# Performance work log

Hardware: AMD Instinct MI355X
Metric: run time of the kernel (lower is better)

Reference implementation:

```python
import jax, jax.numpy as jnp
import numpy as np

B, S, D, O = 8, 2048, 1024, 1024  # batch, seq_len, state_dim(=input_dim), output_dim


def setup_inputs() -> dict:
    key = jax.random.key(0)
    k_in, k_a, k_bc = jax.random.split(key, 3)
    inputs = jax.random.normal(k_in, (B, S, D), dtype=jnp.float32)
    # Stable diagonal transition (|A| < 1) so the 2048-step recurrence stays bounded.
    A = jax.random.uniform(k_a, (D,), minval=-0.99, maxval=0.99, dtype=jnp.float32)
    BC = jax.random.normal(k_bc, (D, O), dtype=jnp.float32) / D
    return {"inputs": inputs, "A": A, "BC": BC}


def reference(inputs, A, BC):
    # Diagonal LTI recurrence: h_t = A * h_{t-1} + x_t ; out_t = h_t @ BC
    # h0 = zeros (the module's h0 Parameter is initialized to zeros).
    x_tfirst = jnp.swapaxes(inputs, 0, 1)  # [S, B, D]

    def step(h, x_t):
        h = h * A + x_t
        return h, h

    h0 = jnp.zeros((inputs.shape[0], A.shape[0]), dtype=inputs.dtype)
    _, hs = jax.lax.scan(step, h0, x_tfirst)  # hs: [S, B, D]
    # Single fused projection over all timesteps instead of per-step matmuls.
    out = jnp.einsum('sbd,do->bso', hs, BC)  # [B, S, O]
    return out
```

## Files before the change

### kernel.cpp

```cpp
#include <hip/hip_runtime.h>
#include <hip/hip_bf16.h>

#define BB 8
#define SS 2048
#define DD 1024
#define OO 1024
#define MM (BB * SS)
#define KK DD
#define NN OO
#define CC 64
#define LL 32

typedef __bf16 bf16x8 __attribute__((ext_vector_type(8)));
typedef __bf16 bf16x2 __attribute__((ext_vector_type(2)));
typedef float floatx4 __attribute__((ext_vector_type(4)));

__device__ __forceinline__ float2 fma2(float2 h, float2 a, float2 v) {
    h.x = fmaf(h.x, a.x, v.x);
    h.y = fmaf(h.y, a.y, v.y);
    return h;
}

__global__ __launch_bounds__(512) void prep(const float* __restrict__ x,
                                            const float* __restrict__ A,
                                            float* __restrict__ carry,
                                            const float* __restrict__ BC,
                                            __bf16* __restrict__ BCt) {
    __shared__ float tile[32][33];
    const int id = blockIdx.x;
    if (id < BB * CC) {
        const int c = id & (CC - 1);
        const int b = id >> 6;
        const int i2 = threadIdx.x;
        const float2 a = ((const float2*)A)[i2];
        const float2* xp = (const float2*)(x + ((size_t)b * SS + (size_t)c * LL) * DD) + i2;
        float2 h = make_float2(0.f, 0.f);
#pragma unroll
        for (int t0 = 0; t0 < LL; t0 += 8) {
            float2 v[8];
#pragma unroll
            for (int u = 0; u < 8; ++u) v[u] = xp[(size_t)(t0 + u) * (DD / 2)];
#pragma unroll
            for (int u = 0; u < 8; ++u) h = fma2(h, a, v[u]);
        }
        ((float2*)carry)[((size_t)b * CC + c) * (DD / 2) + i2] = h;
    } else {
        const int t = id - BB * CC;
        const int o0 = (t & 31) * 32;
        const int d0 = (t >> 5) * 32;
        const int tx = threadIdx.x & 31;
        const int ty = threadIdx.x >> 5;
#pragma unroll
        for (int i = 0; i < 2; ++i) {
            const int dd = ty + i * 16;
            tile[dd][tx] = BC[(size_t)(d0 + dd) * OO + o0 + tx];
        }
        __syncthreads();
#pragma unroll
        for (int i = 0; i < 2; ++i) {
            const int oo = ty + i * 16;
            BCt[(size_t)(o0 + oo) * DD + d0 + tx] = (__bf16)tile[tx][oo];
        }
    }
}

__global__ __launch_bounds__(512) void scan_emit(const float* __restrict__ x,
                                                 const float* __restrict__ A,
                                                 const float* __restrict__ carry,
                                                 __bf16* __restrict__ hs) {
    const int id = blockIdx.x;
    const int c = id & (CC - 1);
    const int b = id >> 6;
    const int i2 = threadIdx.x;
    const float2 a = ((const float2*)A)[i2];
    float2 aL = a;
#pragma unroll
    for (int i = 0; i < 5; ++i) { aL.x *= aL.x; aL.y *= aL.y; }
    float2 h = make_float2(0.f, 0.f);
    const float2* cp = (const float2*)carry + (size_t)b * CC * (DD / 2) + i2;
    int j = 0;
    for (; j + 8 <= c; j += 8) {
        float2 cv[8];
#pragma unroll
        for (int u = 0; u < 8; ++u) cv[u] = cp[(size_t)(j + u) * (DD / 2)];
#pragma unroll
        for (int u = 0; u < 8; ++u) h = fma2(h, aL, cv[u]);
    }
    for (; j < c; ++j) h = fma2(h, aL, cp[(size_t)j * (DD / 2)]);

    const size_t base = ((size_t)b * SS + (size_t)c * LL) * DD;
    const float2* xp = (const float2*)(x + base) + i2;
    bf16x2* hp = (bf16x2*)(hs + base) + i2;
#pragma unroll
    for (int t0 = 0; t0 < LL; t0 += 8) {
        float2 v[8];
#pragma unroll
        for (int u = 0; u < 8; ++u) v[u] = xp[(size_t)(t0 + u) * (DD / 2)];
#pragma unroll
        for (int u = 0; u < 8; ++u) {
            h = fma2(h, a, v[u]);
            bf16x2 o;
            o[0] = (__bf16)h.x; o[1] = (__bf16)h.y;
            hp[(size_t)(t0 + u) * (DD / 2)] = o;
        }
    }
}

#define GTM 256
#define GTN 256
#define GTK 64
#define GNT (KK / GTK)

__device__ __forceinline__ void async16(void* lds, const void* g) {
    __builtin_amdgcn_global_load_lds(
        (__attribute__((address_space(1))) void*)(void*)g,
        (__attribute__((address_space(3))) void*)lds, 16, 0, 0);
}

#define MEMFENCE asm volatile("" ::: "memory")
#define BARRIER do { MEMFENCE; __builtin_amdgcn_s_barrier(); MEMFENCE; } while (0)
#define VMCNT0 asm volatile("s_waitcnt vmcnt(0)" ::: "memory")

__global__ __launch_bounds__(512, 2) void gemm_bt(const __bf16* __restrict__ Am,
                                                  const __bf16* __restrict__ Bt,
                                                  float* __restrict__ C) {
    __shared__ __align__(16) __bf16 As[2][GTM * GTK];
    __shared__ __align__(16) __bf16 Bs[2][GTN * GTK];

    const int tid = threadIdx.x;
    const int wave = tid >> 6;
    const int lane = tid & 63;
    const int wm = (wave >> 2) * 128;
    const int wn = (wave & 3) * 64;
    const int lanelo = lane & 15;
    const int quad = lane >> 4;

    const int bid = blockIdx.x;
    const int xcd = bid & 7;
    const int loc = bid >> 3;
    const int tile_m = (xcd * 8 + (loc >> 2)) * GTM;
    const int tile_n = (loc & 3) * GTN;

    const __bf16* gsrc[4][2];
    int ldsoff[4][2];
#pragma unroll
    for (int a = 0; a < 2; ++a)
#pragma unroll
        for (int u = 0; u < 2; ++u) {
            const int idx = a * 1024 + u * 512 + tid;
            const int rho = idx >> 3, qs = idx & 7;
            const int rl = rho & 127;
            const int r = (rl >> 6) * 128 + a * 64 + (rl & 63);
            const int qg = qs ^ (rho & 7);
            gsrc[a * 3][u] = Am + (size_t)(tile_m + r) * KK + qg * 8;
            ldsoff[a * 3][u] = idx * 8;
        }
#pragma unroll
    for (int b = 0; b < 2; ++b)
#pragma unroll
        for (int u = 0; u < 2; ++u) {
            const int idx = b * 1024 + u * 512 + tid;
            const int rho = idx >> 3, qs = idx & 7;
            const int rl = rho & 127;
            const int r = (rl >> 5) * 64 + b * 32 + (rl & 31);
            const int qg = qs ^ (rho & 7);
            gsrc[1 + b][u] = Bt + (size_t)(tile_n + r) * KK + qg * 8;
            ldsoff[1 + b][u] = idx * 8;
        }

    auto stage = [&](int p, int bufi, int koff) {
        __bf16* base = (p == 0 || p == 3) ? As[bufi] : Bs[bufi];
#pragma unroll
        for (int u = 0; u < 2; ++u)
            async16(base + ldsoff[p][u], gsrc[p][u] + koff);
    };

    floatx4 acc[8][4];
#pragma unroll
    for (int i = 0; i < 8; ++i)
#pragma unroll
        for (int j = 0; j < 4; ++j) acc[i][j] = (floatx4){0.f, 0.f, 0.f, 0.f};

    bf16x8 af[4][2];
    bf16x8 bv[2][2][2];

    auto read_a = [&](const __bf16* as, int mh) {
#pragma unroll
        for (int il = 0; il < 4; ++il)
#pragma unroll
            for (int kk = 0; kk < 2; ++kk) {
                const int rho = mh * 128 + (wm >> 1) + il * 16 + lanelo;
                af[il][kk] = *(const bf16x8*)(as + rho * 64 + (((kk * 4 + quad) ^ (lanelo & 7)) * 8));
            }
    };
    auto read_b = [&](const __bf16* bs, int nh) {
#pragma unroll
        for (int jl = 0; jl < 2; ++jl)
#pragma unroll
            for (int kk = 0; kk < 2; ++kk) {
                const int rho = nh * 128 + (wn >> 1) + jl * 16 + lanelo;
                bv[nh][jl][kk] = *(const bf16x8*)(bs + rho * 64 + (((kk * 4 + quad) ^ (lanelo & 7)) * 8));
            }
    };
    auto mfma16 = [&](int mh, int nh) {
        __builtin_amdgcn_s_setprio(1);
#pragma unroll
        for (int il = 0; il < 4; ++il)
#pragma unroll
            for (int jl = 0; jl < 2; ++jl)
#pragma unroll
                for (int kk = 0; kk < 2; ++kk)
                    acc[mh * 4 + il][nh * 2 + jl] = __builtin_amdgcn_mfma_f32_16x16x32_bf16(
                        af[il][kk], bv[nh][jl][kk], acc[mh * 4 + il][nh * 2 + jl], 0, 0, 0);
        __builtin_amdgcn_s_setprio(0);
    };
    auto store_q = [&](int mh, int nh) {
#pragma unroll
        for (int il = 0; il < 4; ++il) {
            const int row = tile_m + wm + (mh * 4 + il) * 16 + quad * 4;
#pragma unroll
            for (int r = 0; r < 4; ++r) {
                float* crow = C + (size_t)(row + r) * NN + tile_n + wn + lanelo;
#pragma unroll
                for (int jl = 0; jl < 2; ++jl)
                    crow[(nh * 2 + jl) * 16] = acc[mh * 4 + il][nh * 2 + jl][r];
            }
        }
    };

    stage(0, 0, 0);
    stage(3, 0, 0);
    stage(1, 0, 0);
    stage(2, 0, 0);

    for (int t = 0; t < GNT - 1; ++t) {
        const int cur = t & 1, nxt = cur ^ 1;
        const __bf16* as = As[cur];
        const __bf16* bs = Bs[cur];
        const int ko = (t + 1) * GTK;

        VMCNT0;
        BARRIER;

        stage(0, nxt, ko);
        stage(3, nxt, ko);
        stage(1, nxt, ko);
        stage(2, nxt, ko);

        read_a(as, 0);
        read_b(bs, 0);
        mfma16(0, 0);

        read_b(bs, 1);
        mfma16(0, 1);

        read_a(as, 1);
        mfma16(1, 1);

        mfma16(1, 0);
    }

    {
        const __bf16* as = As[(GNT - 1) & 1];
        const __bf16* bs = Bs[(GNT - 1) & 1];
        VMCNT0;
        BARRIER;
        read_a(as, 0);
        read_b(bs, 0);
        mfma16(0, 0);
        read_b(bs, 1);
        mfma16(0, 1);
        store_q(0, 0);
        read_a(as, 1);
        mfma16(1, 1);
        store_q(0, 1);
        mfma16(1, 0);
        store_q(1, 0);
        store_q(1, 1);
    }
}

extern "C" void kernel_launch(void* const* d_in, const int* in_sizes, int n_in,
                              void* d_out, int out_size, void* d_ws, size_t ws_size,
                              hipStream_t stream) {
    const float* x  = (const float*)d_in[0];
    const float* A  = (const float*)d_in[1];
    const float* BC = (const float*)d_in[2];
    float* out = (float*)d_out;

    char* ws = (char*)d_ws;
    __bf16* hs   = (__bf16*)ws;
    float* carry = (float*)(ws + 33554432);
    __bf16* BCt  = (__bf16*)(ws + 33554432 + 2097152);

    prep<<<dim3(BB * CC + 1024), 512, 0, stream>>>(x, A, carry, BC, BCt);
    scan_emit<<<dim3(BB * CC), 512, 0, stream>>>(x, A, carry, hs);
    gemm_bt<<<dim3(MM / GTM * (NN / GTN)), 512, 0, stream>>>(hs, BCt, out);
}
```

Before: 166.7 us.

## Fuse chunk-carry and scan-emit kernels with inter-block flag synchronization

Merges the prep and scan_emit kernels into one launch. Each chunk block computes its local carry, publishes a flag, then spin-waits on the flags of earlier chunks in the same batch before combining carries and emitting hs. The BC transpose blocks now handle four tiles each. This removes one kernel launch and keeps the x chunk warm in cache between the two passes, at the cost of spin-waiting, a reliance on all 512 scan blocks being co-resident to avoid deadlock, and a memset of flags placed in the output buffer.

```diff
diff --git a/kernel.cpp b/kernel.cpp
--- a/kernel.cpp
+++ b/kernel.cpp
@@ -21,58 +21,69 @@
     return h;
 }
 
-__global__ __launch_bounds__(512) void prep(const float* __restrict__ x,
-                                            const float* __restrict__ A,
-                                            float* __restrict__ carry,
-                                            const float* __restrict__ BC,
-                                            __bf16* __restrict__ BCt) {
+__global__ __launch_bounds__(512) void scan_fused(const float* __restrict__ x,
+                                                  const float* __restrict__ A,
+                                                  float* __restrict__ carry,
+                                                  const float* __restrict__ BC,
+                                                  __bf16* __restrict__ BCt,
+                                                  __bf16* __restrict__ hs,
+                                                  unsigned int* __restrict__ flags) {
     __shared__ float tile[32][33];
     const int id = blockIdx.x;
-    if (id < BB * CC) {
-        const int c = id & (CC - 1);
-        const int b = id >> 6;
-        const int i2 = threadIdx.x;
-        const float2 a = ((const float2*)A)[i2];
-        const float2* xp = (const float2*)(x + ((size_t)b * SS + (size_t)c * LL) * DD) + i2;
-        float2 h = make_float2(0.f, 0.f);
-#pragma unroll
-        for (int t0 = 0; t0 < LL; t0 += 8) {
-            float2 v[8];
-#pragma unroll
-            for (int u = 0; u < 8; ++u) v[u] = xp[(size_t)(t0 + u) * (DD / 2)];
-#pragma unroll
-            for (int u = 0; u < 8; ++u) h = fma2(h, a, v[u]);
-        }
-        ((float2*)carry)[((size_t)b * CC + c) * (DD / 2) + i2] = h;
-    } else {
-        const int t = id - BB * CC;
-        const int o0 = (t & 31) * 32;
-        const int d0 = (t >> 5) * 32;
+    if (id >= BB * CC) {
         const int tx = threadIdx.x & 31;
         const int ty = threadIdx.x >> 5;
 #pragma unroll
-        for (int i = 0; i < 2; ++i) {
-            const int dd = ty + i * 16;
-            tile[dd][tx] = BC[(size_t)(d0 + dd) * OO + o0 + tx];
-        }
-        __syncthreads();
-#pragma unroll
-        for (int i = 0; i < 2; ++i) {
-            const int oo = ty + i * 16;
-            BCt[(size_t)(o0 + oo) * DD + d0 + tx] = (__bf16)tile[tx][oo];
-        }
-    }
-}
-
-__global__ __launch_bounds__(512) void scan_emit(const float* __restrict__ x,
-                                                 const float* __restrict__ A,
-                                                 const float* __restrict__ carry,
-                                                 __bf16* __restrict__ hs) {
-    const int id = blockIdx.x;
+        for (int w = 0; w < 4; ++w) {
+            const int t = (id - BB * CC) * 4 + w;
+            const int o0 = (t & 31) * 32;
+            const int d0 = (t >> 5) * 32;
+            __syncthreads();
+#pragma unroll
+            for (int i = 0; i < 2; ++i) {
+                const int dd = ty + i * 16;
+                tile[dd][tx] = BC[(size_t)(d0 + dd) * OO + o0 + tx];
+            }
+            __syncthreads();
+#pragma unroll
+            for (int i = 0; i < 2; ++i) {
+                const int oo = ty + i * 16;
+                BCt[(size_t)(o0 + oo) * DD + d0 + tx] = (__bf16)tile[tx][oo];
+            }
+        }
+        return;
+    }
+
     const int c = id & (CC - 1);
     const int b = id >> 6;
     const int i2 = threadIdx.x;
     const float2 a = ((const float2*)A)[i2];
+    const size_t base = ((size_t)b * SS + (size_t)c * LL) * DD;
+    const float2* xp = (const float2*)(x + base) + i2;
+
+    {
+        float2 h = make_float2(0.f, 0.f);
+#pragma unroll
+        for (int t0 = 0; t0 < LL; t0 += 8) {
+            float2 v[8];
+#pragma unroll
+            for (int u = 0; u < 8; ++u) v[u] = xp[(size_t)(t0 + u) * (DD / 2)];
+#pragma unroll
+            for (int u = 0; u < 8; ++u) h = fma2(h, a, v[u]);
+        }
+        ((float2*)carry)[((size_t)b * CC + c) * (DD / 2) + i2] = h;
+    }
+    __threadfence();
+    __syncthreads();
+    if (threadIdx.x == 0) atomicExch(&flags[id], 1u);
+
+    if ((int)threadIdx.x < c) {
+        while (atomicAdd(&flags[(b << 6) + threadIdx.x], 0u) == 0u)
+            __builtin_amdgcn_s_sleep(2);
+    }
+    __syncthreads();
+    __threadfence();
+
     float2 aL = a;
 #pragma unroll
     for (int i = 0; i < 5; ++i) { aL.x *= aL.x; aL.y *= aL.y; }
@@ -88,8 +99,6 @@
     }
     for (; j < c; ++j) h = fma2(h, aL, cp[(size_t)j * (DD / 2)]);
 
-    const size_t base = ((size_t)b * SS + (size_t)c * LL) * DD;
-    const float2* xp = (const float2*)(x + base) + i2;
     bf16x2* hp = (bf16x2*)(hs + base) + i2;
 #pragma unroll
     for (int t0 = 0; t0 < LL; t0 += 8) {
@@ -293,7 +302,9 @@
     float* carry = (float*)(ws + 33554432);
     __bf16* BCt  = (__bf16*)(ws + 33554432 + 2097152);
 
-    prep<<<dim3(BB * CC + 1024), 512, 0, stream>>>(x, A, carry, BC, BCt);
-    scan_emit<<<dim3(BB * CC), 512, 0, stream>>>(x, A, carry, hs);
+    unsigned int* flags = (unsigned int*)d_out;
+    hipMemsetAsync(flags, 0, BB * CC * sizeof(unsigned int), stream);
+
+    scan_fused<<<dim3(BB * CC + 256), 512, 0, stream>>>(x, A, carry, BC, BCt, hs, flags);
     gemm_bt<<<dim3(MM / GTM * (NN / GTN)), 512, 0, stream>>>(hs, BCt, out);
 }
```

Result: slower. 425.3 us (+155.1%).

## Restructure GEMM main loop into finer-grained interleaved load/compute stages

Applied to the files above, without the earlier changes.

Replaces the per-K-tile full vmcnt(0) wait and single barrier with a schedule that splits each tile's global-to-LDS staging into four quarter loads. These are interleaved with the four MFMA quadrants, using partial vmcnt waits, extra barriers and sched_barrier fences. Quarter loads for the tile after next go into the current buffer once its parts are consumed, so loads run about 1.5 tiles ahead. The aim is to hide global load latency behind MFMA work, at the cost of many more barriers per iteration and a fragile correctness argument about buffer reuse.

```diff
diff --git a/kernel.cpp b/kernel.cpp
--- a/kernel.cpp
+++ b/kernel.cpp
@@ -119,7 +119,11 @@
 
 #define MEMFENCE asm volatile("" ::: "memory")
 #define BARRIER do { MEMFENCE; __builtin_amdgcn_s_barrier(); MEMFENCE; } while (0)
+#define VMCNT6 asm volatile("s_waitcnt vmcnt(6)" ::: "memory")
+#define VMCNT4 asm volatile("s_waitcnt vmcnt(4)" ::: "memory")
 #define VMCNT0 asm volatile("s_waitcnt vmcnt(0)" ::: "memory")
+#define LGKM0  asm volatile("s_waitcnt lgkmcnt(0)" ::: "memory")
+#define SCHED0 __builtin_amdgcn_sched_barrier(0)
 
 __global__ __launch_bounds__(512, 2) void gemm_bt(const __bf16* __restrict__ Am,
                                                   const __bf16* __restrict__ Bt,
@@ -229,35 +233,82 @@
     };
 
     stage(0, 0, 0);
+    stage(2, 0, 0);
+    stage(1, 0, 0);
     stage(3, 0, 0);
-    stage(1, 0, 0);
-    stage(2, 0, 0);
-
-    for (int t = 0; t < GNT - 1; ++t) {
-        const int cur = t & 1, nxt = cur ^ 1;
-        const __bf16* as = As[cur];
-        const __bf16* bs = Bs[cur];
-        const int ko = (t + 1) * GTK;
-
-        VMCNT0;
-        BARRIER;
-
-        stage(0, nxt, ko);
-        stage(3, nxt, ko);
-        stage(1, nxt, ko);
-        stage(2, nxt, ko);
-
+    stage(0, 1, GTK);
+    stage(2, 1, GTK);
+    VMCNT4;
+    BARRIER;
+
+    for (int t = 0; t < GNT - 2; ++t) {
+        const int cb = t & 1, nb = cb ^ 1;
+        const __bf16* as = As[cb];
+        const __bf16* bs = Bs[cb];
+        const int ko1 = (t + 1) * GTK;
+        const int ko2 = (t + 2) * GTK;
+
+        stage(1, nb, ko1);
         read_a(as, 0);
         read_b(bs, 0);
+        VMCNT6; BARRIER;
+        LGKM0; SCHED0;
         mfma16(0, 0);
-
+        BARRIER;
+
+        stage(3, nb, ko1);
         read_b(bs, 1);
+        VMCNT6; BARRIER;
+        LGKM0; SCHED0;
         mfma16(0, 1);
-
+        BARRIER;
+
+        stage(0, cb, ko2);
         read_a(as, 1);
+        VMCNT6; BARRIER;
+        LGKM0; SCHED0;
         mfma16(1, 1);
-
+        BARRIER;
+
+        stage(2, cb, ko2);
+        VMCNT6; BARRIER;
+        SCHED0;
         mfma16(1, 0);
+        BARRIER;
+    }
+
+    {
+        const int t = GNT - 2;
+        const int cb = t & 1, nb = cb ^ 1;
+        const __bf16* as = As[cb];
+        const __bf16* bs = Bs[cb];
+        const int ko1 = (t + 1) * GTK;
+
+        stage(1, nb, ko1);
+        read_a(as, 0);
+        read_b(bs, 0);
+        VMCNT6; BARRIER;
+        LGKM0; SCHED0;
+        mfma16(0, 0);
+        BARRIER;
+
+        stage(3, nb, ko1);
+        read_b(bs, 1);
+        VMCNT6; BARRIER;
+        LGKM0; SCHED0;
+        mfma16(0, 1);
+        BARRIER;
+
+        read_a(as, 1);
+        VMCNT6; BARRIER;
+        LGKM0; SCHED0;
+        mfma16(1, 1);
+        BARRIER;
+
+        VMCNT6; BARRIER;
+        SCHED0;
+        mfma16(1, 0);
+        BARRIER;
     }
 
     {
@@ -267,11 +318,14 @@
         BARRIER;
         read_a(as, 0);
         read_b(bs, 0);
+        LGKM0; SCHED0;
         mfma16(0, 0);
         read_b(bs, 1);
+        LGKM0; SCHED0;
         mfma16(0, 1);
         store_q(0, 0);
         read_a(as, 1);
+        LGKM0; SCHED0;
         mfma16(1, 1);
         store_q(0, 1);
         mfma16(1, 0);
```

Result: slower. 172.0 us (+3.1%).

## Fuse chunk scan into GEMM A-tile staging, drop bf16 hs buffer

Applied to the files above, without the earlier changes.

The materialized bf16 hidden-state tensor is removed. A small kernel now writes only the per-chunk starting states. Inside the GEMM, each wave loads 32 timesteps of fp32 input for a 64-wide K slice, runs the recurrence in registers and writes bf16 values straight into the swizzled LDS A tile. This avoids writing and re-reading the 32MB hs buffer, but each of the four N-tile blocks per M tile now re-reads fp32 x (twice the bytes of the bf16 hs) and redoes the scan. The scan runs as synchronous loads in the GEMM loop instead of async staging, which may stall MFMA issue.

```diff
diff --git a/kernel.cpp b/kernel.cpp
--- a/kernel.cpp
+++ b/kernel.cpp
@@ -12,7 +12,6 @@
 #define LL 32
 
 typedef __bf16 bf16x8 __attribute__((ext_vector_type(8)));
-typedef __bf16 bf16x2 __attribute__((ext_vector_type(2)));
 typedef float floatx4 __attribute__((ext_vector_type(4)));
 
 __device__ __forceinline__ float2 fma2(float2 h, float2 a, float2 v) {
@@ -64,10 +63,9 @@
     }
 }
 
-__global__ __launch_bounds__(512) void scan_emit(const float* __restrict__ x,
-                                                 const float* __restrict__ A,
-                                                 const float* __restrict__ carry,
-                                                 __bf16* __restrict__ hs) {
+__global__ __launch_bounds__(512) void prefix_k(const float* __restrict__ A,
+                                                const float* __restrict__ carry,
+                                                float* __restrict__ P) {
     const int id = blockIdx.x;
     const int c = id & (CC - 1);
     const int b = id >> 6;
@@ -87,23 +85,7 @@
         for (int u = 0; u < 8; ++u) h = fma2(h, aL, cv[u]);
     }
     for (; j < c; ++j) h = fma2(h, aL, cp[(size_t)j * (DD / 2)]);
-
-    const size_t base = ((size_t)b * SS + (size_t)c * LL) * DD;
-    const float2* xp = (const float2*)(x + base) + i2;
-    bf16x2* hp = (bf16x2*)(hs + base) + i2;
-#pragma unroll
-    for (int t0 = 0; t0 < LL; t0 += 8) {
-        float2 v[8];
-#pragma unroll
-        for (int u = 0; u < 8; ++u) v[u] = xp[(size_t)(t0 + u) * (DD / 2)];
-#pragma unroll
-        for (int u = 0; u < 8; ++u) {
-            h = fma2(h, a, v[u]);
-            bf16x2 o;
-            o[0] = (__bf16)h.x; o[1] = (__bf16)h.y;
-            hp[(size_t)(t0 + u) * (DD / 2)] = o;
-        }
-    }
+    ((float2*)P)[(size_t)id * (DD / 2) + i2] = h;
 }
 
 #define GTM 256
@@ -120,8 +102,11 @@
 #define MEMFENCE asm volatile("" ::: "memory")
 #define BARRIER do { MEMFENCE; __builtin_amdgcn_s_barrier(); MEMFENCE; } while (0)
 #define VMCNT0 asm volatile("s_waitcnt vmcnt(0)" ::: "memory")
-
-__global__ __launch_bounds__(512, 2) void gemm_bt(const __bf16* __restrict__ Am,
+#define LGKM0  asm volatile("s_waitcnt lgkmcnt(0)" ::: "memory")
+
+__global__ __launch_bounds__(512, 2) void gemm_bt(const float* __restrict__ x,
+                                                  const float* __restrict__ Av,
+                                                  const float* __restrict__ P,
                                                   const __bf16* __restrict__ Bt,
                                                   float* __restrict__ C) {
     __shared__ __align__(16) __bf16 As[2][GTM * GTK];
@@ -141,38 +126,51 @@
     const int tile_m = (xcd * 8 + (loc >> 2)) * GTM;
     const int tile_n = (loc & 3) * GTN;
 
-    const __bf16* gsrc[4][2];
-    int ldsoff[4][2];
-#pragma unroll
-    for (int a = 0; a < 2; ++a)
+    const __bf16* gsrcB[2][2];
+    int ldsoffB[2][2];
+#pragma unroll
+    for (int b2 = 0; b2 < 2; ++b2)
 #pragma unroll
         for (int u = 0; u < 2; ++u) {
-            const int idx = a * 1024 + u * 512 + tid;
+            const int idx = b2 * 1024 + u * 512 + tid;
             const int rho = idx >> 3, qs = idx & 7;
             const int rl = rho & 127;
-            const int r = (rl >> 6) * 128 + a * 64 + (rl & 63);
+            const int r = (rl >> 5) * 64 + b2 * 32 + (rl & 31);
             const int qg = qs ^ (rho & 7);
-            gsrc[a * 3][u] = Am + (size_t)(tile_m + r) * KK + qg * 8;
-            ldsoff[a * 3][u] = idx * 8;
-        }
-#pragma unroll
-    for (int b = 0; b < 2; ++b)
-#pragma unroll
-        for (int u = 0; u < 2; ++u) {
-            const int idx = b * 1024 + u * 512 + tid;
-            const int rho = idx >> 3, qs = idx & 7;
-            const int rl = rho & 127;
-            const int r = (rl >> 5) * 64 + b * 32 + (rl & 31);
-            const int qg = qs ^ (rho & 7);
-            gsrc[1 + b][u] = Bt + (size_t)(tile_n + r) * KK + qg * 8;
-            ldsoff[1 + b][u] = idx * 8;
-        }
-
-    auto stage = [&](int p, int bufi, int koff) {
-        __bf16* base = (p == 0 || p == 3) ? As[bufi] : Bs[bufi];
-#pragma unroll
-        for (int u = 0; u < 2; ++u)
-            async16(base + ldsoff[p][u], gsrc[p][u] + koff);
+            gsrcB[b2][u] = Bt + (size_t)(tile_n + r) * KK + qg * 8;
+            ldsoffB[b2][u] = idx * 8;
+        }
+
+    auto stageB = [&](int bufi, int koff) {
+#pragma unroll
+        for (int b2 = 0; b2 < 2; ++b2)
+#pragma unroll
+            for (int u = 0; u < 2; ++u)
+                async16(&Bs[bufi][ldsoffB[b2][u]], gsrcB[b2][u] + koff);
+    };
+
+    const int dq = lane >> 3, dlow = lane & 7;
+    const int pcw = (tile_m >> 5) + wave;
+    const float* xrow = x + (size_t)(tile_m + wave * 32) * DD + lane;
+
+    auto scanA = [&](int kt, int bufi) {
+        const int d0 = kt * 64;
+        const float a_d = Av[d0 + lane];
+        float h = P[(size_t)pcw * DD + d0 + lane];
+        const float* xp = xrow + d0;
+        __bf16* as = &As[bufi][wave * 32 * 64];
+#pragma unroll
+        for (int g = 0; g < 4; ++g) {
+            float v[8];
+#pragma unroll
+            for (int u = 0; u < 8; ++u) v[u] = xp[(size_t)(g * 8 + u) * DD];
+#pragma unroll
+            for (int u = 0; u < 8; ++u) {
+                const int t = g * 8 + u;
+                h = fmaf(h, a_d, v[u]);
+                as[t * 64 + ((dq ^ u) << 3) + dlow] = (__bf16)h;
+            }
+        }
     };
 
     floatx4 acc[8][4];
@@ -189,8 +187,8 @@
         for (int il = 0; il < 4; ++il)
 #pragma unroll
             for (int kk = 0; kk < 2; ++kk) {
-                const int rho = mh * 128 + (wm >> 1) + il * 16 + lanelo;
-                af[il][kk] = *(const bf16x8*)(as + rho * 64 + (((kk * 4 + quad) ^ (lanelo & 7)) * 8));
+                const int row = wm + (mh * 4 + il) * 16 + lanelo;
+                af[il][kk] = *(const bf16x8*)(as + row * 64 + (((kk * 4 + quad) ^ (lanelo & 7)) * 8));
             }
     };
     auto read_b = [&](const __bf16* bs, int nh) {
@@ -228,55 +226,44 @@
         }
     };
 
-    stage(0, 0, 0);
-    stage(3, 0, 0);
-    stage(1, 0, 0);
-    stage(2, 0, 0);
-
-    for (int t = 0; t < GNT - 1; ++t) {
+    stageB(0, 0);
+    scanA(0, 0);
+
+    for (int t = 0; t < GNT; ++t) {
+        VMCNT0;
+        LGKM0;
+        BARRIER;
         const int cur = t & 1, nxt = cur ^ 1;
         const __bf16* as = As[cur];
         const __bf16* bs = Bs[cur];
-        const int ko = (t + 1) * GTK;
-
-        VMCNT0;
-        BARRIER;
-
-        stage(0, nxt, ko);
-        stage(3, nxt, ko);
-        stage(1, nxt, ko);
-        stage(2, nxt, ko);
-
-        read_a(as, 0);
-        read_b(bs, 0);
-        mfma16(0, 0);
-
-        read_b(bs, 1);
-        mfma16(0, 1);
-
-        read_a(as, 1);
-        mfma16(1, 1);
-
-        mfma16(1, 0);
-    }
-
-    {
-        const __bf16* as = As[(GNT - 1) & 1];
-        const __bf16* bs = Bs[(GNT - 1) & 1];
-        VMCNT0;
-        BARRIER;
-        read_a(as, 0);
-        read_b(bs, 0);
-        mfma16(0, 0);
-        read_b(bs, 1);
-        mfma16(0, 1);
-        store_q(0, 0);
-        read_a(as, 1);
-        mfma16(1, 1);
-        store_q(0, 1);
-        mfma16(1, 0);
-        store_q(1, 0);
-        store_q(1, 1);
+
+        if (t + 1 < GNT) {
+            stageB(nxt, (t + 1) * GTK);
+
+            read_a(as, 0);
+            read_b(bs, 0);
+            mfma16(0, 0);
+            read_b(bs, 1);
+            mfma16(0, 1);
+            read_a(as, 1);
+            mfma16(1, 1);
+            mfma16(1, 0);
+
+            scanA(t + 1, nxt);
+        } else {
+            read_a(as, 0);
+            read_b(bs, 0);
+            mfma16(0, 0);
+            read_b(bs, 1);
+            mfma16(0, 1);
+            store_q(0, 0);
+            read_a(as, 1);
+            mfma16(1, 1);
+            store_q(0, 1);
+            mfma16(1, 0);
+            store_q(1, 0);
+            store_q(1, 1);
+        }
     }
 }
 
@@ -289,11 +276,11 @@
     float* out = (float*)d_out;
 
     char* ws = (char*)d_ws;
-    __bf16* hs   = (__bf16*)ws;
+    float* P     = (float*)ws;
     float* carry = (float*)(ws + 33554432);
     __bf16* BCt  = (__bf16*)(ws + 33554432 + 2097152);
 
     prep<<<dim3(BB * CC + 1024), 512, 0, stream>>>(x, A, carry, BC, BCt);
-    scan_emit<<<dim3(BB * CC), 512, 0, stream>>>(x, A, carry, hs);
-    gemm_bt<<<dim3(MM / GTM * (NN / GTN)), 512, 0, stream>>>(hs, BCt, out);
-}
+    prefix_k<<<dim3(BB * CC), 512, 0, stream>>>(A, carry, P);
+    gemm_bt<<<dim3(MM / GTM * (NN / GTN)), 512, 0, stream>>>(x, A, P, BCt, out);
+}
```

After: 173.5 us. +4.1%, slower.
